# Optimization experiments

Hardware: AMD Instinct MI355X
Metric: run time of the kernel (lower is better)

Reference implementation:

```python
import jax, jax.numpy as jnp
import numpy as np

B = 2097152  # flattened batch of 3x3 rotation matrices

def setup_inputs() -> dict:
    key = jax.random.key(0)
    k1, k2 = jax.random.split(key)
    # scale by 0.1 so cos=(trace(m1 m2^T)-1)/2 stays strictly inside (-1,1)
    pred_rot = jax.random.normal(k1, (B, 3, 3), dtype=jnp.float32) * 0.1
    gt_rot = jax.random.normal(k2, (B, 3, 3), dtype=jnp.float32) * 0.1
    return {"pred_rot": pred_rot, "gt_rot": gt_rot}

def reference(pred_rot, gt_rot):
    m1 = pred_rot.reshape(-1, 3, 3)
    m2 = gt_rot.reshape(-1, 3, 3)
    # trace(m1 @ m2^T) == sum(m1 * m2) elementwise -> avoid the bmm
    cos = (jnp.einsum('bij,bij->b', m1, m2) - 1.0) * 0.5
    cos = jnp.clip(cos, -1.0, 1.0)  # min with +1, max with -1
    theta = jnp.arccos(cos)
    return jnp.mean(theta)  # reduction='mean'
```

## Files before the change

kernel.cpp:

```cpp
#include <hip/hip_runtime.h>
#include <math.h>


#define TPB 256
#define MPB 512
#define FLOATS_PER_IN 4608
#define F4_PER_IN 1152

typedef const __attribute__((address_space(1))) float4 g_f4;
typedef __attribute__((address_space(3))) float4 l_f4;

__global__ __launch_bounds__(TPB) void geo_kernel(
    const float* __restrict__ a, const float* __restrict__ b,
    float* __restrict__ out, float invM, int M)
{
    __shared__ float lds[2 * FLOATS_PER_IN];
    __shared__ float wsum[TPB / 64];

    const int tid = threadIdx.x;
    const long long tile_m0 = (long long)blockIdx.x * MPB;
    float sum = 0.0f;

    if (tile_m0 + MPB <= M) {
        const float4* a4 = (const float4*)(a + tile_m0 * 9);
        const float4* b4 = (const float4*)(b + tile_m0 * 9);
        const int wave_base = tid & ~63;

        #pragma unroll
        for (int k = 0; k < 4; ++k) {
            const int idx = k * 256 + tid;
            const int uni = k * 256 + wave_base;
            __builtin_amdgcn_global_load_lds((g_f4*)(a4 + idx),
                (l_f4*)((float4*)lds + uni), 16, 0, 0);
            __builtin_amdgcn_global_load_lds((g_f4*)(b4 + idx),
                (l_f4*)((float4*)lds + F4_PER_IN + uni), 16, 0, 0);
        }
        if (tid < 128) {
            const int idx = 1024 + tid;
            const int uni = 1024 + wave_base;
            __builtin_amdgcn_global_load_lds((g_f4*)(a4 + idx),
                (l_f4*)((float4*)lds + uni), 16, 0, 0);
            __builtin_amdgcn_global_load_lds((g_f4*)(b4 + idx),
                (l_f4*)((float4*)lds + F4_PER_IN + uni), 16, 0, 0);
        }
        __syncthreads();

        const float* al = lds;
        const float* bl = lds + FLOATS_PER_IN;
        #pragma unroll
        for (int c = 0; c < 2; ++c) {
            float d = 0.0f;
            #pragma unroll
            for (int j = 0; j < 9; ++j)
                d = fmaf(al[9 * tid + 2304 * c + j],
                         bl[9 * tid + 2304 * c + j], d);
            float cv = fminf(1.0f, fmaxf(-1.0f, (d - 1.0f) * 0.5f));
            sum += acosf(cv);
        }
    } else {
        for (int c = 0; c < 2; ++c) {
            long long m = tile_m0 + tid + 256 * c;
            if (m < M) {
                float d = 0.0f;
                for (int j = 0; j < 9; ++j)
                    d = fmaf(a[m * 9 + j], b[m * 9 + j], d);
                float cv = fminf(1.0f, fmaxf(-1.0f, (d - 1.0f) * 0.5f));
                sum += acosf(cv);
            }
        }
    }

    #pragma unroll
    for (int off = 32; off > 0; off >>= 1)
        sum += __shfl_down(sum, off, 64);
    const int lane = tid & 63;
    const int wid  = tid >> 6;
    if (lane == 0) wsum[wid] = sum;
    __syncthreads();
    if (tid == 0) {
        float s = 0.0f;
        #pragma unroll
        for (int i = 0; i < TPB / 64; ++i) s += wsum[i];
        atomicAdd(out, s * invM);
    }
}

extern "C" void kernel_launch(void* const* d_in, const int* in_sizes, int n_in,
                              void* d_out, int out_size, void* d_ws, size_t ws_size,
                              hipStream_t stream) {
    const float* a = (const float*)d_in[0];
    const float* b = (const float*)d_in[1];
    float* out = (float*)d_out;

    const int n = in_sizes[0];
    const int M = n / 9;

    const int grid = (M + MPB - 1) / MPB;

    hipMemsetAsync(out, 0, (size_t)out_size * sizeof(float), stream);
    geo_kernel<<<grid, TPB, 0, stream>>>(a, b, out, 1.0f / (float)M, M);
}
```

Before: 178.2 us.

## Multiply inputs in registers and stage only products in LDS, larger tiles

Replaces the async global-to-LDS loads of both inputs with coalesced float4 register loads. The elementwise products are computed immediately and only the product tile goes to LDS, which halves LDS footprint and traffic per matrix. The tile doubles to 1024 matrices per block with 4 matrices per thread, giving fewer blocks and atomics but more work per thread. The risk is losing the direct-to-LDS async path and possibly lowering occupancy from the larger per-thread work.

```diff
diff --git a/kernel.cpp b/kernel.cpp
--- a/kernel.cpp
+++ b/kernel.cpp
@@ -3,18 +3,15 @@
 
 
 #define TPB 256
-#define MPB 512
-#define FLOATS_PER_IN 4608
-#define F4_PER_IN 1152
-
-typedef const __attribute__((address_space(1))) float4 g_f4;
-typedef __attribute__((address_space(3))) float4 l_f4;
+#define MPB 1024
+#define F_PER_TILE 9216
+#define F4_PER_TILE 2304
 
 __global__ __launch_bounds__(TPB) void geo_kernel(
     const float* __restrict__ a, const float* __restrict__ b,
     float* __restrict__ out, float invM, int M)
 {
-    __shared__ float lds[2 * FLOATS_PER_IN];
+    __shared__ float prod[F_PER_TILE];
     __shared__ float wsum[TPB / 64];
 
     const int tid = threadIdx.x;
@@ -22,43 +19,31 @@
     float sum = 0.0f;
 
     if (tile_m0 + MPB <= M) {
-        const float4* a4 = (const float4*)(a + tile_m0 * 9);
-        const float4* b4 = (const float4*)(b + tile_m0 * 9);
-        const int wave_base = tid & ~63;
-
+        const float4* __restrict__ a4 = (const float4*)(a + tile_m0 * 9);
+        const float4* __restrict__ b4 = (const float4*)(b + tile_m0 * 9);
         #pragma unroll
-        for (int k = 0; k < 4; ++k) {
-            const int idx = k * 256 + tid;
-            const int uni = k * 256 + wave_base;
-            __builtin_amdgcn_global_load_lds((g_f4*)(a4 + idx),
-                (l_f4*)((float4*)lds + uni), 16, 0, 0);
-            __builtin_amdgcn_global_load_lds((g_f4*)(b4 + idx),
-                (l_f4*)((float4*)lds + F4_PER_IN + uni), 16, 0, 0);
-        }
-        if (tid < 128) {
-            const int idx = 1024 + tid;
-            const int uni = 1024 + wave_base;
-            __builtin_amdgcn_global_load_lds((g_f4*)(a4 + idx),
-                (l_f4*)((float4*)lds + uni), 16, 0, 0);
-            __builtin_amdgcn_global_load_lds((g_f4*)(b4 + idx),
-                (l_f4*)((float4*)lds + F4_PER_IN + uni), 16, 0, 0);
+        for (int k = 0; k < 9; ++k) {
+            const int i = k * TPB + tid;
+            float4 va = a4[i];
+            float4 vb = b4[i];
+            float4 p;
+            p.x = va.x * vb.x; p.y = va.y * vb.y;
+            p.z = va.z * vb.z; p.w = va.w * vb.w;
+            ((float4*)prod)[i] = p;
         }
         __syncthreads();
-
-        const float* al = lds;
-        const float* bl = lds + FLOATS_PER_IN;
         #pragma unroll
-        for (int c = 0; c < 2; ++c) {
-            float d = 0.0f;
-            #pragma unroll
-            for (int j = 0; j < 9; ++j)
-                d = fmaf(al[9 * tid + 2304 * c + j],
-                         bl[9 * tid + 2304 * c + j], d);
+        for (int c = 0; c < 4; ++c) {
+            const int base = 9 * (tid + 256 * c);
+            float d = ((prod[base + 0] + prod[base + 1]) +
+                       (prod[base + 2] + prod[base + 3])) +
+                      ((prod[base + 4] + prod[base + 5]) +
+                       (prod[base + 6] + prod[base + 7])) + prod[base + 8];
             float cv = fminf(1.0f, fmaxf(-1.0f, (d - 1.0f) * 0.5f));
             sum += acosf(cv);
         }
     } else {
-        for (int c = 0; c < 2; ++c) {
+        for (int c = 0; c < 4; ++c) {
             long long m = tile_m0 + tid + 256 * c;
             if (m < M) {
                 float d = 0.0f;
```

New measurement: 167.0 us. 1.07x faster.
